# Kernel optimization log

Hardware: AMD Instinct MI355X
Metric: run time of the kernel (lower is better)

## Reference

```python
import jax, jax.numpy as jnp
import numpy as np

N_NODES = 50000
N_EDGES = 800000
FEAT = 128
HID = 64
N_CLS = 12


def setup_inputs() -> dict:
    key = jax.random.key(0)
    ks = jax.random.split(key, 8)
    x = jax.random.normal(ks[0], (N_NODES, FEAT), dtype=jnp.float32)
    edge_index = jax.random.randint(ks[1], (2, N_EDGES), 0, N_NODES, dtype=jnp.int64)
    s1 = 1.0 / np.sqrt(FEAT)
    s2 = 1.0 / np.sqrt(HID)
    W1 = jax.random.uniform(ks[2], (FEAT, HID), jnp.float32, -s1, s1)
    b1 = jnp.zeros((HID,), jnp.float32)
    W2 = jax.random.uniform(ks[3], (HID, HID), jnp.float32, -s2, s2)
    b2 = jnp.zeros((HID,), jnp.float32)
    Wfc = jax.random.uniform(ks[4], (HID, N_CLS), jnp.float32, -s2, s2)
    bfc = jax.random.uniform(ks[5], (N_CLS,), jnp.float32, -s2, s2)
    return {"x": x, "edge_index": edge_index, "W1": W1, "b1": b1,
            "W2": W2, "b2": b2, "Wfc": Wfc, "bfc": bfc}


def gcn_conv(x, W, b, src, dst, n_nodes):
    """PyG GCNConv: symmetric-normalized aggregation with self-loops.
    out_i = sum_{j in N(i)} (xW)_j / sqrt(d_i d_j) + (xW)_i / d_i + b,
    where d = in-degree + 1 (self loop)."""
    xw = x @ W  # [N, out] -- transform before propagate (PyG order)
    deg = jnp.zeros((n_nodes,), x.dtype).at[dst].add(1.0) + 1.0
    dinv = jax.lax.rsqrt(deg)
    norm = dinv[src] * dinv[dst]  # [E]
    agg = jax.ops.segment_sum(xw[src] * norm[:, None], dst, num_segments=n_nodes)
    agg = agg + xw * (dinv * dinv)[:, None]  # self-loop term
    return agg + b


def reference(x, edge_index, W1, b1, W2, b2, Wfc, bfc):
    n = x.shape[0]
    src, dst = edge_index[0], edge_index[1]
    h = jax.nn.relu(gcn_conv(x, W1, b1, src, dst, n))
    h = jax.nn.relu(gcn_conv(h, W2, b2, src, dst, n))
    return h @ Wfc + bfc  # [N, num_content_categories]
```

## Files before the change

### kernel.cpp

```cpp
#include <hip/hip_runtime.h>
#include <hip/hip_fp16.h>


#define CAP   64
#define NBUK  196
#define ET    4096
#define NB    196

typedef unsigned short u16;
typedef unsigned long long u64;

__global__ __launch_bounds__(256) void k_hist(const int* __restrict__ dst,
                                              int* __restrict__ blkcnt, int E) {
    __shared__ int hist[NBUK];
    const int tid = threadIdx.x, blk = blockIdx.x;
    for (int i = tid; i < NBUK; i += 256) hist[i] = 0;
    __syncthreads();
    const int e0 = blk * ET;
    if (e0 + ET <= E) {
        const int4* d4 = (const int4*)(dst + e0);
#pragma unroll
        for (int j = 0; j < ET / 1024; j++) {
            int4 d = d4[j * 256 + tid];
            atomicAdd(&hist[(unsigned)d.x >> 8], 1);
            atomicAdd(&hist[(unsigned)d.y >> 8], 1);
            atomicAdd(&hist[(unsigned)d.z >> 8], 1);
            atomicAdd(&hist[(unsigned)d.w >> 8], 1);
        }
    } else {
        for (int j = 0; j < ET / 256; j++) {
            int e = e0 + j * 256 + tid;
            if (e < E) atomicAdd(&hist[(unsigned)dst[e] >> 8], 1);
        }
    }
    __syncthreads();
    for (int b = tid; b < NBUK; b += 256) blkcnt[b * NB + blk] = hist[b];
}

__global__ __launch_bounds__(256) void k_scanA(int* __restrict__ blkcnt,
                                               int* __restrict__ btot) {
    __shared__ int s[256];
    const int t = threadIdx.x, b = blockIdx.x;
    int v = (t < NB) ? blkcnt[b * NB + t] : 0;
    s[t] = v;
    __syncthreads();
#pragma unroll
    for (int d = 1; d < 256; d <<= 1) {
        int u = (t >= d) ? s[t - d] : 0;
        __syncthreads();
        s[t] += u;
        __syncthreads();
    }
    if (t < NB) blkcnt[b * NB + t] = s[t] - v;
    if (t == 255) btot[b] = s[255];
}

__device__ __forceinline__ void local_bucket_scan(const int* __restrict__ btot,
                                                  int* bb, int tid) {
    if (tid < 256) bb[tid] = (tid < NBUK) ? btot[tid] : 0;
    __syncthreads();
#pragma unroll
    for (int d = 1; d < 256; d <<= 1) {
        int u = 0;
        if (tid < 256 && tid >= d) u = bb[tid - d];
        __syncthreads();
        if (tid < 256) bb[tid] += u;
        __syncthreads();
    }
    if (tid < 256) bb[tid] -= (tid < NBUK) ? btot[tid] : 0;
    __syncthreads();
}

__global__ __launch_bounds__(256) void k_scatter(const int* __restrict__ src,
                                                 const int* __restrict__ dst,
                                                 const int* __restrict__ blkcnt,
                                                 const int* __restrict__ btot,
                                                 unsigned* __restrict__ eb, int E) {
    __shared__ int bb[256];
    __shared__ int cur[NBUK];
    const int tid = threadIdx.x, blk = blockIdx.x;
    local_bucket_scan(btot, bb, tid);
    for (int i = tid; i < NBUK; i += 256) cur[i] = blkcnt[i * NB + blk] + bb[i];
    __syncthreads();
    const int e0 = blk * ET;
    if (e0 + ET <= E) {
        const int4* s4 = (const int4*)(src + e0);
        const int4* d4 = (const int4*)(dst + e0);
#pragma unroll
        for (int j = 0; j < ET / 1024; j++) {
            int4 sv = s4[j * 256 + tid];
            int4 dv = d4[j * 256 + tid];
            unsigned u0 = ((unsigned)dv.x << 16) | (unsigned)sv.x;
            unsigned u1 = ((unsigned)dv.y << 16) | (unsigned)sv.y;
            unsigned u2 = ((unsigned)dv.z << 16) | (unsigned)sv.z;
            unsigned u3 = ((unsigned)dv.w << 16) | (unsigned)sv.w;
            eb[atomicAdd(&cur[u0 >> 24], 1)] = u0;
            eb[atomicAdd(&cur[u1 >> 24], 1)] = u1;
            eb[atomicAdd(&cur[u2 >> 24], 1)] = u2;
            eb[atomicAdd(&cur[u3 >> 24], 1)] = u3;
        }
    } else {
        for (int j = 0; j < ET / 256; j++) {
            int e = e0 + j * 256 + tid;
            if (e < E) {
                unsigned d = (unsigned)dst[e];
                unsigned u = (d << 16) | (unsigned)src[e];
                eb[atomicAdd(&cur[d >> 8], 1)] = u;
            }
        }
    }
}

__global__ __launch_bounds__(1024) void k_buildb(const unsigned* __restrict__ eb,
                                                 const int* __restrict__ btot,
                                                 u16* __restrict__ csr,
                                                 int* __restrict__ cnt, int n) {
    __shared__ int bb[256];
    __shared__ u16 lcsr[256 * CAP];
    __shared__ int cur[256];
    const int tid = threadIdx.x, b = blockIdx.x;
    local_bucket_scan(btot, bb, tid);
    if (tid < 256) cur[tid] = 0;
    __syncthreads();
    const int e0 = bb[b], e1 = bb[b] + btot[b];
    for (int e = e0 + tid; e < e1; e += 1024) {
        unsigned u = __builtin_nontemporal_load(eb + e);
        int ld = (int)((u >> 16) & 255u);
        int p = atomicAdd(&cur[ld], 1);
        if (p < CAP) lcsr[ld * CAP + p] = (u16)(u & 0xffffu);
    }
    __syncthreads();
    const int node0 = b * 256;
    for (int i = tid; i < 256 * CAP / 8; i += 1024) {
        int r = i / (CAP / 8), q = i % (CAP / 8);
        int c = cur[r] < CAP ? cur[r] : CAP;
        uint4 v = *(uint4*)&lcsr[r * CAP + q * 8];
        if (q * 8 >= c) v = make_uint4(0, 0, 0, 0);
        *(uint4*)&csr[(size_t)(node0 + r) * CAP + q * 8] = v;
    }
    if (tid < 256 && node0 + tid < n) cnt[node0 + tid] = cur[tid];
}

template <int K, bool IS_HALF, typename TIN>
__global__ __launch_bounds__(256) void k_gemm(const TIN* __restrict__ X,
                                              const float* __restrict__ W,
                                              const int* __restrict__ cnt,
                                              __half* __restrict__ Y, int n) {
    constexpr int KC = 64;
    constexpr int XS = KC + 4;
    __shared__ float ws[KC * 64];
    __shared__ float xs[64 * XS];
    const int tid = threadIdx.x;
    const int tx = tid & 15;
    const int ty = tid >> 4;
    const int row0 = blockIdx.x * 64;

    float acc[4][4];
#pragma unroll
    for (int r = 0; r < 4; r++)
#pragma unroll
        for (int c = 0; c < 4; c++) acc[r][c] = 0.f;

#pragma unroll 1
    for (int kc = 0; kc < K; kc += KC) {
        for (int i = tid; i < KC * 16; i += 256) {
            int kk = i >> 4, c4 = i & 15;
            *(float4*)&ws[kk * 64 + 4 * c4] = *(const float4*)&W[(kc + kk) * 64 + 4 * c4];
        }
        if (IS_HALF) {
            for (int i = tid; i < 64 * (KC / 8); i += 256) {
                int r = i >> 3, q = i & 7;
                uint4 u = make_uint4(0, 0, 0, 0);
                int row = row0 + r;
                if (row < n) u = *(const uint4*)&X[(size_t)row * K + kc + 8 * q];
                float2 f0 = __half22float2(*(__half2*)&u.x);
                float2 f1 = __half22float2(*(__half2*)&u.y);
                float2 f2 = __half22float2(*(__half2*)&u.z);
                float2 f3 = __half22float2(*(__half2*)&u.w);
                *(float4*)&xs[r * XS + 8 * q]     = make_float4(f0.x, f0.y, f1.x, f1.y);
                *(float4*)&xs[r * XS + 8 * q + 4] = make_float4(f2.x, f2.y, f3.x, f3.y);
            }
        } else {
            for (int i = tid; i < 64 * (KC / 4); i += 256) {
                int r = i / (KC / 4), q = i % (KC / 4);
                float4 v = make_float4(0.f, 0.f, 0.f, 0.f);
                int row = row0 + r;
                if (row < n) v = *(const float4*)&((const float*)X)[(size_t)row * K + kc + 4 * q];
                *(float4*)&xs[r * XS + 4 * q] = v;
            }
        }
        __syncthreads();

#pragma unroll 2
        for (int q = 0; q < KC / 4; q++) {
            float4 xv[4];
#pragma unroll
            for (int r = 0; r < 4; r++)
                xv[r] = *(const float4*)&xs[(ty + 16 * r) * XS + 4 * q];
#pragma unroll
            for (int kk = 0; kk < 4; kk++) {
                float4 wv = *(const float4*)&ws[(4 * q + kk) * 64 + 4 * tx];
#pragma unroll
                for (int r = 0; r < 4; r++) {
                    float xval = (kk == 0) ? xv[r].x : (kk == 1) ? xv[r].y
                               : (kk == 2) ? xv[r].z : xv[r].w;
                    acc[r][0] = fmaf(xval, wv.x, acc[r][0]);
                    acc[r][1] = fmaf(xval, wv.y, acc[r][1]);
                    acc[r][2] = fmaf(xval, wv.z, acc[r][2]);
                    acc[r][3] = fmaf(xval, wv.w, acc[r][3]);
                }
            }
        }
        __syncthreads();
    }

#pragma unroll
    for (int r = 0; r < 4; r++) {
        int row = row0 + ty + 16 * r;
        if (row < n) {
            float d = rsqrtf((float)cnt[row] + 1.0f);
            __half2* yh = (__half2*)&Y[(size_t)row * 64 + 4 * tx];
            yh[0] = __floats2half2_rn(acc[r][0] * d, acc[r][1] * d);
            yh[1] = __floats2half2_rn(acc[r][2] * d, acc[r][3] * d);
        }
    }
}

__device__ __forceinline__ float4 gather_node(const __half* __restrict__ y,
                                              const u16* __restrict__ lst,
                                              int deg, int c4) {
    float4 a0 = make_float4(0.f, 0.f, 0.f, 0.f);
    float4 a1 = make_float4(0.f, 0.f, 0.f, 0.f);
    int i = 0;
    for (; i + 16 <= deg; i += 16) {
        const u64* lp = (const u64*)(lst + i);
        u64 q0 = __builtin_nontemporal_load(lp);
        u64 q1 = __builtin_nontemporal_load(lp + 1);
        u64 q2 = __builtin_nontemporal_load(lp + 2);
        u64 q3 = __builtin_nontemporal_load(lp + 3);
        unsigned idx[16];
#pragma unroll
        for (int t = 0; t < 4; t++) {
            idx[t]      = (unsigned)((q0 >> (16 * t)) & 0xffffu);
            idx[t + 4]  = (unsigned)((q1 >> (16 * t)) & 0xffffu);
            idx[t + 8]  = (unsigned)((q2 >> (16 * t)) & 0xffffu);
            idx[t + 12] = (unsigned)((q3 >> (16 * t)) & 0xffffu);
        }
        uint2 v[16];
#pragma unroll
        for (int t = 0; t < 16; t++) v[t] = *(const uint2*)&y[(size_t)idx[t] * 64 + 4 * c4];
#pragma unroll
        for (int t = 0; t < 16; t += 2) {
            float2 lo0 = __half22float2(*(__half2*)&v[t].x);
            float2 hi0 = __half22float2(*(__half2*)&v[t].y);
            float2 lo1 = __half22float2(*(__half2*)&v[t + 1].x);
            float2 hi1 = __half22float2(*(__half2*)&v[t + 1].y);
            a0.x += lo0.x; a0.y += lo0.y; a0.z += hi0.x; a0.w += hi0.y;
            a1.x += lo1.x; a1.y += lo1.y; a1.z += hi1.x; a1.w += hi1.y;
        }
    }
    if (i + 8 <= deg) {
        const u64* lp = (const u64*)(lst + i);
        u64 q0 = __builtin_nontemporal_load(lp);
        u64 q1 = __builtin_nontemporal_load(lp + 1);
        unsigned idx[8];
#pragma unroll
        for (int t = 0; t < 4; t++) {
            idx[t]     = (unsigned)((q0 >> (16 * t)) & 0xffffu);
            idx[t + 4] = (unsigned)((q1 >> (16 * t)) & 0xffffu);
        }
        uint2 v[8];
#pragma unroll
        for (int t = 0; t < 8; t++) v[t] = *(const uint2*)&y[(size_t)idx[t] * 64 + 4 * c4];
#pragma unroll
        for (int t = 0; t < 8; t += 2) {
            float2 lo0 = __half22float2(*(__half2*)&v[t].x);
            float2 hi0 = __half22float2(*(__half2*)&v[t].y);
            float2 lo1 = __half22float2(*(__half2*)&v[t + 1].x);
            float2 hi1 = __half22float2(*(__half2*)&v[t + 1].y);
            a0.x += lo0.x; a0.y += lo0.y; a0.z += hi0.x; a0.w += hi0.y;
            a1.x += lo1.x; a1.y += lo1.y; a1.z += hi1.x; a1.w += hi1.y;
        }
        i += 8;
    }
    if (i + 4 <= deg) {
        u64 q0 = __builtin_nontemporal_load((const u64*)(lst + i));
        unsigned idx[4];
#pragma unroll
        for (int t = 0; t < 4; t++) idx[t] = (unsigned)((q0 >> (16 * t)) & 0xffffu);
        uint2 v[4];
#pragma unroll
        for (int t = 0; t < 4; t++) v[t] = *(const uint2*)&y[(size_t)idx[t] * 64 + 4 * c4];
#pragma unroll
        for (int t = 0; t < 4; t += 2) {
            float2 lo0 = __half22float2(*(__half2*)&v[t].x);
            float2 hi0 = __half22float2(*(__half2*)&v[t].y);
            float2 lo1 = __half22float2(*(__half2*)&v[t + 1].x);
            float2 hi1 = __half22float2(*(__half2*)&v[t + 1].y);
            a0.x += lo0.x; a0.y += lo0.y; a0.z += hi0.x; a0.w += hi0.y;
            a1.x += lo1.x; a1.y += lo1.y; a1.z += hi1.x; a1.w += hi1.y;
        }
        i += 4;
    }
    for (; i < deg; i++) {
        uint2 vv = *(const uint2*)&y[(size_t)lst[i] * 64 + 4 * c4];
        float2 lo = __half22float2(*(__half2*)&vv.x);
        float2 hi = __half22float2(*(__half2*)&vv.y);
        a0.x += lo.x; a0.y += lo.y; a0.z += hi.x; a0.w += hi.y;
    }
    return make_float4(a0.x + a1.x, a0.y + a1.y, a0.z + a1.z, a0.w + a1.w);
}

__global__ __launch_bounds__(256) void k_agg1(const __half* __restrict__ y,
                                              const u16* __restrict__ csr,
                                              const int* __restrict__ cnt,
                                              const float* __restrict__ bias,
                                              __half* __restrict__ h1, int n) {
    const int tid = threadIdx.x;
    const int c4 = tid & 15;
    const int node = blockIdx.x * 16 + (tid >> 4);
    if (node >= n) return;
    int deg_raw = cnt[node];
    int deg = deg_raw > CAP ? CAP : deg_raw;
    float4 acc = gather_node(y, csr + node * CAP, deg, c4);
    uint2 sv = *(const uint2*)&y[(size_t)node * 64 + 4 * c4];
    float2 slo = __half22float2(*(__half2*)&sv.x);
    float2 shi = __half22float2(*(__half2*)&sv.y);
    float d = rsqrtf((float)deg_raw + 1.0f);
    float4 bv = *(const float4*)&bias[4 * c4];
    float v0 = fmaxf(fmaf(d, acc.x + slo.x, bv.x), 0.f);
    float v1 = fmaxf(fmaf(d, acc.y + slo.y, bv.y), 0.f);
    float v2 = fmaxf(fmaf(d, acc.z + shi.x, bv.z), 0.f);
    float v3 = fmaxf(fmaf(d, acc.w + shi.y, bv.w), 0.f);
    __half2 o0 = __floats2half2_rn(v0, v1);
    __half2 o1 = __floats2half2_rn(v2, v3);
    u64 packed = (u64)(*(unsigned*)&o0) | ((u64)(*(unsigned*)&o1) << 32);
    __builtin_nontemporal_store(packed, (u64*)&h1[(size_t)node * 64 + 4 * c4]);
}

__global__ __launch_bounds__(256) void k_agg2fc(const __half* __restrict__ y,
                                                const u16* __restrict__ csr,
                                                const int* __restrict__ cnt,
                                                const float* __restrict__ bias,
                                                const float* __restrict__ Wfc,
                                                const float* __restrict__ bfc,
                                                float* __restrict__ out, int n) {
    __shared__ float wf[12 * 64];
    __shared__ float bf[12];
    const int tid = threadIdx.x;
    for (int i = tid; i < 12 * 64; i += 256) {
        int c = i >> 6, k = i & 63;
        wf[i] = Wfc[k * 12 + c];
    }
    if (tid < 12) bf[tid] = bfc[tid];
    __syncthreads();

    const int c4 = tid & 15;
    const int node = blockIdx.x * 16 + (tid >> 4);
    if (node >= n) return;
    int deg_raw = cnt[node];
    int deg = deg_raw > CAP ? CAP : deg_raw;
    float4 acc = gather_node(y, csr + node * CAP, deg, c4);
    uint2 sv = *(const uint2*)&y[(size_t)node * 64 + 4 * c4];
    float2 slo = __half22float2(*(__half2*)&sv.x);
    float2 shi = __half22float2(*(__half2*)&sv.y);
    float d = rsqrtf((float)deg_raw + 1.0f);
    float4 bv = *(const float4*)&bias[4 * c4];
    float v0 = fmaxf(fmaf(d, acc.x + slo.x, bv.x), 0.f);
    float v1 = fmaxf(fmaf(d, acc.y + slo.y, bv.y), 0.f);
    float v2 = fmaxf(fmaf(d, acc.z + shi.x, bv.z), 0.f);
    float v3 = fmaxf(fmaf(d, acc.w + shi.y, bv.w), 0.f);

    float res = 0.f;
#pragma unroll
    for (int c = 0; c < 12; c++) {
        float4 wv = *(const float4*)&wf[c * 64 + 4 * c4];
        float p = v0 * wv.x + v1 * wv.y + v2 * wv.z + v3 * wv.w;
        p += __shfl_xor(p, 1);
        p += __shfl_xor(p, 2);
        p += __shfl_xor(p, 4);
        p += __shfl_xor(p, 8);
        if (c4 == c) res = p + bf[c];
    }
    if (c4 < 12) out[(size_t)node * 12 + c4] = res;
}

extern "C" void kernel_launch(void* const* d_in, const int* in_sizes, int n_in,
                              void* d_out, int out_size, void* d_ws, size_t ws_size,
                              hipStream_t stream) {
    const float* x   = (const float*)d_in[0];
    const int*   ei  = (const int*)d_in[1];
    const float* W1  = (const float*)d_in[2];
    const float* b1  = (const float*)d_in[3];
    const float* W2  = (const float*)d_in[4];
    const float* b2  = (const float*)d_in[5];
    const float* Wfc = (const float*)d_in[6];
    const float* bfc = (const float*)d_in[7];
    float* out = (float*)d_out;

    const int n = in_sizes[0] / 128;
    const int E = in_sizes[1] / 2;
    const int* src = ei;
    const int* dst = ei + E;
    const int nblk = (E + ET - 1) / ET;

    char* w = (char*)d_ws;
    unsigned* eb  = (unsigned*)w;  w += (size_t)((E + 63) / 64) * 64 * 4;
    int* blkcnt   = (int*)w;       w += (size_t)NBUK * NB * 4 + 256;
    int* btot     = (int*)w;       w += 256 * 4;
    int* cnt      = (int*)w;       w += (size_t)((n + 63) / 64) * 64 * 4;
    u16* csr      = (u16*)w;       w += (size_t)NBUK * 256 * CAP * 2;
    __half* y     = (__half*)w;    w += (size_t)n * 64 * 2;
    __half* h1    = (__half*)w;

    k_hist   <<<dim3(nblk), dim3(256), 0, stream>>>(dst, blkcnt, E);
    k_scanA  <<<dim3(NBUK), dim3(256), 0, stream>>>(blkcnt, btot);
    k_scatter<<<dim3(nblk), dim3(256), 0, stream>>>(src, dst, blkcnt, btot, eb, E);
    k_buildb <<<dim3(NBUK), dim3(1024), 0, stream>>>(eb, btot, csr, cnt, n);
    k_gemm<128, false, float><<<dim3((n + 63) / 64), dim3(256), 0, stream>>>(x, W1, cnt, y, n);
    k_agg1   <<<dim3((n + 15) / 16), dim3(256), 0, stream>>>(y, csr, cnt, b1, h1, n);
    k_gemm<64, true, __half><<<dim3((n + 63) / 64), dim3(256), 0, stream>>>(h1, W2, cnt, y, n);
    k_agg2fc <<<dim3((n + 15) / 16), dim3(256), 0, stream>>>(y, csr, cnt, b2, Wfc, bfc, out, n);
}
```

Measured before the change: 184.7 us.

## Use fp16 MFMA for dense transforms with pre-transposed half weights

Replaces the scalar FP32 FMA tiled GEMM with a kernel using the 16x16x32 f16 MFMA instruction. A new prep kernel converts W1 and W2 to transposed fp16 copies in the workspace, and x is converted to fp16 when staged into shared memory. This cuts the ALU cost of the two dense transforms, at the price of fp16 rounding on x and W1 and scalar half stores instead of vectorized writes. Adds one extra small kernel launch.

```diff
diff --git a/kernel.cpp b/kernel.cpp
--- a/kernel.cpp
+++ b/kernel.cpp
@@ -9,6 +9,25 @@
 
 typedef unsigned short u16;
 typedef unsigned long long u64;
+typedef _Float16 f16;
+typedef _Float16 f16x8 __attribute__((ext_vector_type(8)));
+typedef float f32x4 __attribute__((ext_vector_type(4)));
+
+__global__ __launch_bounds__(256) void k_prep(const float* __restrict__ W1,
+                                              const float* __restrict__ W2,
+                                              f16* __restrict__ W1t,
+                                              f16* __restrict__ W2t) {
+    int i = blockIdx.x * 256 + threadIdx.x;
+    if (i < 128 * 64) {
+        int k = i >> 6, nn = i & 63;
+        W1t[nn * 128 + k] = (f16)W1[k * 64 + nn];
+    }
+    int j = i - 128 * 64;
+    if (j >= 0 && j < 64 * 64) {
+        int k = j >> 6, nn = j & 63;
+        W2t[nn * 64 + k] = (f16)W2[k * 64 + nn];
+    }
+}
 
 __global__ __launch_bounds__(256) void k_hist(const int* __restrict__ dst,
                                               int* __restrict__ blkcnt, int E) {
@@ -143,87 +162,73 @@
 
 template <int K, bool IS_HALF, typename TIN>
 __global__ __launch_bounds__(256) void k_gemm(const TIN* __restrict__ X,
-                                              const float* __restrict__ W,
+                                              const f16* __restrict__ Wt,
                                               const int* __restrict__ cnt,
                                               __half* __restrict__ Y, int n) {
-    constexpr int KC = 64;
-    constexpr int XS = KC + 4;
-    __shared__ float ws[KC * 64];
-    __shared__ float xs[64 * XS];
+    constexpr int KS = K + 8;
+    __shared__ f16 xsh[64 * KS];
+    __shared__ f16 wsh[64 * KS];
     const int tid = threadIdx.x;
-    const int tx = tid & 15;
-    const int ty = tid >> 4;
     const int row0 = blockIdx.x * 64;
 
-    float acc[4][4];
+    for (int i = tid; i < 64 * (K / 8); i += 256) {
+        int nn = i / (K / 8), kq = i % (K / 8);
+        *(uint4*)&wsh[nn * KS + 8 * kq] = *(const uint4*)&Wt[nn * K + 8 * kq];
+    }
+    if constexpr (IS_HALF) {
+        const __half* Xh = (const __half*)X;
+        for (int i = tid; i < 64 * (K / 8); i += 256) {
+            int r = i / (K / 8), kq = i % (K / 8);
+            uint4 u = make_uint4(0, 0, 0, 0);
+            int row = row0 + r;
+            if (row < n) u = *(const uint4*)&Xh[(size_t)row * K + 8 * kq];
+            *(uint4*)&xsh[r * KS + 8 * kq] = u;
+        }
+    } else {
+        const float* Xf = (const float*)X;
+        for (int i = tid; i < 64 * (K / 4); i += 256) {
+            int r = i / (K / 4), q4 = i % (K / 4);
+            float4 v = make_float4(0.f, 0.f, 0.f, 0.f);
+            int row = row0 + r;
+            if (row < n) v = *(const float4*)&Xf[(size_t)row * K + 4 * q4];
+            __half2 p0 = __floats2half2_rn(v.x, v.y);
+            __half2 p1 = __floats2half2_rn(v.z, v.w);
+            uint2 o = make_uint2(*(unsigned*)&p0, *(unsigned*)&p1);
+            *(uint2*)&xsh[r * KS + 4 * q4] = o;
+        }
+    }
+    __syncthreads();
+
+    const int wv = tid >> 6;
+    const int lane = tid & 63;
+    const int mn = lane & 15;
+    const int q = lane >> 4;
+
+    f32x4 acc[4] = {{0, 0, 0, 0}, {0, 0, 0, 0}, {0, 0, 0, 0}, {0, 0, 0, 0}};
+    const f16* arow = &xsh[(16 * wv + mn) * KS + 8 * q];
+#pragma unroll
+    for (int s = 0; s < K / 32; s++) {
+        f16x8 A = *(const f16x8*)&arow[32 * s];
+#pragma unroll
+        for (int c = 0; c < 4; c++) {
+            f16x8 B = *(const f16x8*)&wsh[(16 * c + mn) * KS + 32 * s + 8 * q];
+            acc[c] = __builtin_amdgcn_mfma_f32_16x16x32_f16(A, B, acc[c], 0, 0, 0);
+        }
+    }
+
+    const int rowb = row0 + 16 * wv + 4 * q;
+    float dinv[4];
 #pragma unroll
     for (int r = 0; r < 4; r++)
-#pragma unroll
-        for (int c = 0; c < 4; c++) acc[r][c] = 0.f;
-
-#pragma unroll 1
-    for (int kc = 0; kc < K; kc += KC) {
-        for (int i = tid; i < KC * 16; i += 256) {
-            int kk = i >> 4, c4 = i & 15;
-            *(float4*)&ws[kk * 64 + 4 * c4] = *(const float4*)&W[(kc + kk) * 64 + 4 * c4];
-        }
-        if (IS_HALF) {
-            for (int i = tid; i < 64 * (KC / 8); i += 256) {
-                int r = i >> 3, q = i & 7;
-                uint4 u = make_uint4(0, 0, 0, 0);
-                int row = row0 + r;
-                if (row < n) u = *(const uint4*)&X[(size_t)row * K + kc + 8 * q];
-                float2 f0 = __half22float2(*(__half2*)&u.x);
-                float2 f1 = __half22float2(*(__half2*)&u.y);
-                float2 f2 = __half22float2(*(__half2*)&u.z);
-                float2 f3 = __half22float2(*(__half2*)&u.w);
-                *(float4*)&xs[r * XS + 8 * q]     = make_float4(f0.x, f0.y, f1.x, f1.y);
-                *(float4*)&xs[r * XS + 8 * q + 4] = make_float4(f2.x, f2.y, f3.x, f3.y);
-            }
-        } else {
-            for (int i = tid; i < 64 * (KC / 4); i += 256) {
-                int r = i / (KC / 4), q = i % (KC / 4);
-                float4 v = make_float4(0.f, 0.f, 0.f, 0.f);
-                int row = row0 + r;
-                if (row < n) v = *(const float4*)&((const float*)X)[(size_t)row * K + kc + 4 * q];
-                *(float4*)&xs[r * XS + 4 * q] = v;
-            }
-        }
-        __syncthreads();
-
-#pragma unroll 2
-        for (int q = 0; q < KC / 4; q++) {
-            float4 xv[4];
-#pragma unroll
-            for (int r = 0; r < 4; r++)
-                xv[r] = *(const float4*)&xs[(ty + 16 * r) * XS + 4 * q];
-#pragma unroll
-            for (int kk = 0; kk < 4; kk++) {
-                float4 wv = *(const float4*)&ws[(4 * q + kk) * 64 + 4 * tx];
-#pragma unroll
-                for (int r = 0; r < 4; r++) {
-                    float xval = (kk == 0) ? xv[r].x : (kk == 1) ? xv[r].y
-                               : (kk == 2) ? xv[r].z : xv[r].w;
-                    acc[r][0] = fmaf(xval, wv.x, acc[r][0]);
-                    acc[r][1] = fmaf(xval, wv.y, acc[r][1]);
-                    acc[r][2] = fmaf(xval, wv.z, acc[r][2]);
-                    acc[r][3] = fmaf(xval, wv.w, acc[r][3]);
-                }
-            }
-        }
-        __syncthreads();
-    }
-
-#pragma unroll
-    for (int r = 0; r < 4; r++) {
-        int row = row0 + ty + 16 * r;
-        if (row < n) {
-            float d = rsqrtf((float)cnt[row] + 1.0f);
-            __half2* yh = (__half2*)&Y[(size_t)row * 64 + 4 * tx];
-            yh[0] = __floats2half2_rn(acc[r][0] * d, acc[r][1] * d);
-            yh[1] = __floats2half2_rn(acc[r][2] * d, acc[r][3] * d);
-        }
-    }
+        dinv[r] = rsqrtf((float)((rowb + r < n) ? cnt[rowb + r] : 0) + 1.0f);
+#pragma unroll
+    for (int c = 0; c < 4; c++)
+#pragma unroll
+        for (int r = 0; r < 4; r++) {
+            int row = rowb + r;
+            if (row < n)
+                Y[(size_t)row * 64 + 16 * c + mn] = __float2half(acc[c][r] * dinv[r]);
+        }
 }
 
 __device__ __forceinline__ float4 gather_node(const __half* __restrict__ y,
@@ -409,16 +414,19 @@
     int* blkcnt   = (int*)w;       w += (size_t)NBUK * NB * 4 + 256;
     int* btot     = (int*)w;       w += 256 * 4;
     int* cnt      = (int*)w;       w += (size_t)((n + 63) / 64) * 64 * 4;
+    f16* W1t      = (f16*)w;       w += 128 * 64 * 2;
+    f16* W2t      = (f16*)w;       w += 64 * 64 * 2 + 256;
     u16* csr      = (u16*)w;       w += (size_t)NBUK * 256 * CAP * 2;
     __half* y     = (__half*)w;    w += (size_t)n * 64 * 2;
     __half* h1    = (__half*)w;
 
+    k_prep   <<<dim3(48), dim3(256), 0, stream>>>(W1, W2, W1t, W2t);
     k_hist   <<<dim3(nblk), dim3(256), 0, stream>>>(dst, blkcnt, E);
     k_scanA  <<<dim3(NBUK), dim3(256), 0, stream>>>(blkcnt, btot);
     k_scatter<<<dim3(nblk), dim3(256), 0, stream>>>(src, dst, blkcnt, btot, eb, E);
     k_buildb <<<dim3(NBUK), dim3(1024), 0, stream>>>(eb, btot, csr, cnt, n);
-    k_gemm<128, false, float><<<dim3((n + 63) / 64), dim3(256), 0, stream>>>(x, W1, cnt, y, n);
+    k_gemm<128, false, float><<<dim3((n + 63) / 64), dim3(256), 0, stream>>>(x, W1t, cnt, y, n);
     k_agg1   <<<dim3((n + 15) / 16), dim3(256), 0, stream>>>(y, csr, cnt, b1, h1, n);
-    k_gemm<64, true, __half><<<dim3((n + 63) / 64), dim3(256), 0, stream>>>(h1, W2, cnt, y, n);
+    k_gemm<64, true, __half><<<dim3((n + 63) / 64), dim3(256), 0, stream>>>(h1, W2t, cnt, y, n);
     k_agg2fc <<<dim3((n + 15) / 16), dim3(256), 0, stream>>>(y, csr, cnt, b2, Wfc, bfc, out, n);
 }
```

Result: faster. 172.9 us, median of 2 (-6.4%).
